# Kernel optimization log

Measured on AMD Instinct MI355X. Metric: run time of the kernel, lower is better.

## Reference

```python
import jax, jax.numpy as jnp
import numpy as np

B, N, L = 32, 50, 16384  # batch, n_templates, segment length
KT = 4096                # template kernel length


def conv1d(x, w, pad, groups=1):
    # x: [B, Cin, L], w: [Cout, Cin/groups, K] (torch layout)
    return jax.lax.conv_general_dilated(
        x, w, window_strides=(1,), padding=[(pad, pad)],
        dimension_numbers=('NCH', 'OIH', 'NCH'), feature_group_count=groups)


def maxpool3(x):
    # MaxPool1d(kernel=3, stride=3), floor mode (VALID)
    return jax.lax.reduce_window(x, -jnp.inf, jax.lax.max,
                                 (1, 1, 3), (1, 1, 3), 'VALID')


def pad_to(x, m):
    p = (-x.shape[-1]) % m
    pads = ((0, 0),) * (x.ndim - 1) + ((0, p),)
    return jnp.pad(x, pads)


def setup_inputs() -> dict:
    key = jax.random.key(0)
    ks = jax.random.split(key, 12)
    return dict(
        xi=jax.random.normal(ks[0], (B, 2, L), jnp.float32),
        S_t_m12=jax.random.normal(ks[1], (2, 1, L), jnp.float32) * 0.01,
        template=jax.random.normal(ks[2], (N, 2, KT), jnp.float32) * 0.01,
        hh_sqrt=jax.random.uniform(ks[3], (N, 2), jnp.float32) + 0.5,
        W1=jax.random.normal(ks[4], (16, 2, 3), jnp.float32) * 0.1,
        b1=jnp.zeros((16,), jnp.float32),
        W2=jax.random.normal(ks[5], (32, 16, 3), jnp.float32) * 0.1,
        b2=jnp.zeros((32,), jnp.float32),
        W3=jax.random.normal(ks[6], (32, 128), jnp.float32) * 0.1,
        b3=jnp.zeros((32,), jnp.float32),
        W4=jax.random.normal(ks[7], (2, 32), jnp.float32) * 0.1,
        b4=jnp.zeros((2,), jnp.float32),
    )


def reference(xi, S_t_m12, template, hh_sqrt, W1, b1, W2, b2, W3, b3, W4, b4):
    # Whitening matched filter: grouped conv with kernel length L
    y = conv1d(xi, S_t_m12, L - 1, groups=2)          # [B, 2, 2L-1]
    y = pad_to(y, L)                                   # [B, 2, 2L]
    # wrap-fold each channel: reshape(B,2,L).sum over the fold axis
    d_SA = y[:, 0].reshape(-1, 2, L).sum(1)[:, None, :]  # [B,1,L]
    d_SE = y[:, 1].reshape(-1, 2, L).sum(1)[:, None, :]
    h_SA = template[:, 0, :].reshape(-1, 1, KT)          # [N,1,KT]
    h_SE = template[:, 1, :].reshape(-1, 1, KT)
    dh_A = pad_to(conv1d(d_SA, h_SA, KT - 1), L).reshape(-1, N, 2, L).sum(2)  # [B,N,L]
    dh_E = pad_to(conv1d(d_SE, h_SE, KT - 1), L).reshape(-1, N, 2, L).sum(2)
    z = jnp.stack((dh_A, dh_E), -1).transpose(0, 2, 1, 3)  # [B,L,N,2]
    z = z / hh_sqrt                                         # broadcast [N,2]
    z = z.max(axis=1).transpose(0, 2, 1)                    # [B,2,N]
    # small CNN + MLP head
    h = maxpool3(jax.nn.sigmoid(conv1d(z, W1, 0) + b1[None, :, None]))  # [B,16,16]
    h = maxpool3(jax.nn.sigmoid(conv1d(h, W2, 0) + b2[None, :, None]))  # [B,32,4]
    h = h.reshape(h.shape[0], -1)                                        # [B,128]
    h = jax.nn.relu(h @ W3.T + b3)
    return h @ W4.T + b4                                                 # [B,2]
```

## Files before the change

kernel.cpp:

```cpp
#include <hip/hip_runtime.h>
#include <math.h>

#define L_LEN 16384
#define M_LEN 8192
#define KT_LEN 4096
#define BB 32
#define NTPL 50
#define SPEC_STRIDE 8224
#define NSIG 166
#define NT 512
#define PI_F 3.14159265358979323846f
#define C16 0.98078528040323044f
#define S16 0.19509032201612827f

typedef float cf2 __attribute__((ext_vector_type(2)));


__device__ __forceinline__ cf2 cmul(cf2 a, cf2 b) {
    cf2 byx = __builtin_shufflevector(b, b, 1, 0);
    return (cf2){a.x, a.x} * b + (cf2){-a.y, a.y} * byx;
}
__device__ __forceinline__ cf2 cmulc(cf2 a, cf2 b) {
    return a * (cf2){b.x, b.x} + (cf2){a.y, -a.x} * (cf2){b.y, b.y};
}
template<int SIGN>
__device__ __forceinline__ cf2 rot90(cf2 z) {
    return (SIGN < 0) ? (cf2){z.y, -z.x} : (cf2){-z.y, z.x};
}
template<int SIGN>
__device__ __forceinline__ cf2 ldT(const cf2* __restrict__ T, int idx) {
    cf2 t = T[idx];
    if (SIGN > 0) t.y = -t.y;
    return t;
}

__device__ __forceinline__ int swz(int i) { return i ^ (((i >> 5) & 15) << 1); }

__device__ __forceinline__ int pos(int f) {
    return ((f & 15) << 9) | (((f >> 4) & 15) << 5) |
           (((f >> 8) & 15) << 1) | ((f >> 12) & 1);
}

template<int SIGN>
__device__ __forceinline__ void dft16(cf2 x[16]) {
    const float S = (SIGN < 0) ? -1.f : 1.f;
    const cf2 w1 = {0.9238795325112867f, S * 0.3826834323650898f};
    const cf2 w2 = {0.7071067811865476f, S * 0.7071067811865476f};
    const cf2 w3 = {0.3826834323650898f, S * 0.9238795325112867f};
    cf2 v[16];
    #pragma unroll
    for (int n1 = 0; n1 < 4; ++n1) {
        cf2 a0 = x[n1], a1 = x[n1+4], a2 = x[n1+8], a3 = x[n1+12];
        cf2 t0 = a0 + a2, t2 = a0 - a2;
        cf2 t1 = a1 + a3, t3 = rot90<SIGN>(a1 - a3);
        cf2 u0 = t0 + t1, u1 = t2 + t3;
        cf2 u2 = t0 - t1, u3 = t2 - t3;
        if (n1 == 1) { u1 = cmul(u1, w1); u2 = cmul(u2, w2); u3 = cmul(u3, w3); }
        else if (n1 == 2) { u1 = cmul(u1, w2); u2 = rot90<SIGN>(u2);
                            u3 = rot90<SIGN>(cmul(u3, w2)); }
        else if (n1 == 3) { u1 = cmul(u1, w3); u2 = rot90<SIGN>(cmul(u2, w2));
                            u3 = -cmul(u3, w1); }
        v[0*4+n1] = u0; v[1*4+n1] = u1; v[2*4+n1] = u2; v[3*4+n1] = u3;
    }
    #pragma unroll
    for (int r = 0; r < 4; ++r) {
        cf2 a0 = v[r*4+0], a1 = v[r*4+1], a2 = v[r*4+2], a3 = v[r*4+3];
        cf2 t0 = a0 + a2, t2 = a0 - a2;
        cf2 t1 = a1 + a3, t3 = rot90<SIGN>(a1 - a3);
        x[r]    = t0 + t1; x[r+4]  = t2 + t3;
        x[r+8]  = t0 - t1; x[r+12] = t2 - t3;
    }
}

template<int SIGN>
__device__ __forceinline__ void butterfly16(cf2* A, const int idx[16], cf2 w1) {
    cf2 x[16];
    #pragma unroll
    for (int n = 0; n < 16; ++n) x[n] = A[idx[n]];
    dft16<SIGN>(x);
    A[idx[0]] = x[0];
    A[idx[1]] = cmul(x[1], w1);
    const cf2 w2 = cmul(w1, w1);
    A[idx[2]] = cmul(x[2], w2);
    const cf2 w3 = cmul(w1, w2);
    A[idx[3]] = cmul(x[3], w3);
    const cf2 w4 = cmul(w2, w2);
    A[idx[4]] = cmul(x[4], w4);
    A[idx[5]] = cmul(x[5], cmul(w1, w4));
    A[idx[6]] = cmul(x[6], cmul(w2, w4));
    A[idx[7]] = cmul(x[7], cmul(w3, w4));
    const cf2 w8 = cmul(w4, w4);
    A[idx[8]]  = cmul(x[8],  w8);
    A[idx[9]]  = cmul(x[9],  cmul(w1, w8));
    A[idx[10]] = cmul(x[10], cmul(w2, w8));
    A[idx[11]] = cmul(x[11], cmul(w3, w8));
    const cf2 w12 = cmul(w4, w8);
    A[idx[12]] = cmul(x[12], w12);
    A[idx[13]] = cmul(x[13], cmul(w1, w12));
    A[idx[14]] = cmul(x[14], cmul(w2, w12));
    A[idx[15]] = cmul(x[15], cmul(w3, w12));
}


__global__ __launch_bounds__(NT, 4)
void fwd_fft_kernel(const float* __restrict__ xi, const float* __restrict__ w,
                    const float* __restrict__ tmpl, cf2* __restrict__ Tw,
                    cf2* __restrict__ spec) {
    __shared__ __attribute__((aligned(16))) cf2 A[M_LEN];
    const int sig = blockIdx.x;
    const int tid = threadIdx.x;

    if (sig >= NSIG) {
        const int k = (sig - NSIG) * NT + tid;
        const double a = -M_PI * (double)k / 8192.0;
        Tw[k] = (cf2){(float)cos(a), (float)sin(a)};
        return;
    }

    const float* src;
    int nre;
    if (sig < 64)      { src = xi   + sig * L_LEN;         nre = L_LEN; }
    else if (sig < 66) { src = w    + (sig - 64) * L_LEN;  nre = L_LEN; }
    else               { src = tmpl + (sig - 66) * KT_LEN; nre = KT_LEN; }
    const bool isW = (sig >= 64 && sig < 66);
    const int nc = nre >> 1;
    const float4* s4 = (const float4*)src;
    const int g0 = tid ^ ((tid >> 4) & 15);
    #pragma unroll
    for (int m = 0; m < 8; ++m) {
        const int u = 2*tid + 1024*m;
        float4 vv = (u < nc) ? s4[tid + 512*m] : make_float4(0.f, 0.f, 0.f, 0.f);
        ((float4*)A)[g0 + 512*m] = vv;
    }
    __syncthreads();

    {
        int idx[16]; const int b0 = swz(tid);
        #pragma unroll
        for (int n = 0; n < 16; ++n) idx[n] = b0 + 512*n;
        float sn, cs; __sincosf(-PI_F * (float)(2*tid) / 8192.f, &sn, &cs);
        butterfly16<-1>(A, idx, (cf2){cs, sn});
    }
    __syncthreads();
    {
        const int blk = tid >> 5, j = tid & 31, jb = blk*512;
        int idx[16];
        #pragma unroll
        for (int n = 0; n < 16; ++n) idx[n] = jb + 32*n + (j ^ (2*n));
        float sn, cs; __sincosf(-PI_F * (float)(32*j) / 8192.f, &sn, &cs);
        butterfly16<-1>(A, idx, (cf2){cs, sn});
    }
    __syncthreads();
    {
        const int blk = tid >> 1, j = tid & 1;
        const int xv = (blk & 15) << 1, b3 = blk*32 + j;
        int idx[16];
        #pragma unroll
        for (int n = 0; n < 16; ++n) idx[n] = b3 + ((2*n) ^ xv);
        cf2 w1 = j ? (cf2){C16, -S16} : (cf2){1.f, 0.f};
        butterfly16<-1>(A, idx, w1);
    }
    __syncthreads();
    #pragma unroll
    for (int m = 0; m < 8; ++m) {
        float4 pq = ((float4*)A)[g0 + 512*m];
        ((float4*)A)[g0 + 512*m] = make_float4(pq.x + pq.z, pq.y + pq.w,
                                               pq.x - pq.z, pq.y - pq.w);
    }
    __syncthreads();

    cf2* out = spec + (size_t)sig * SPEC_STRIDE;
    #pragma unroll
    for (int m = 0; m < 16; ++m) {
        const int f = tid + 512*m;
        const int fb = (M_LEN - f) & (M_LEN - 1);
        cf2 Za = A[swz(pos(f))];
        cf2 Zb = A[swz(pos(fb))];
        cf2 E = (cf2){0.5f*(Za.x + Zb.x), 0.5f*(Za.y - Zb.y)};
        cf2 D = (cf2){Za.x - Zb.x, Za.y + Zb.y};
        cf2 O = (cf2){0.5f*D.y, -0.5f*D.x};
        float sn, cs;
        __sincosf(-PI_F * (float)f / 8192.f, &sn, &cs);
        cf2 val = E + (cf2){cs*O.x - sn*O.y, cs*O.y + sn*O.x};
        if (isW) {
            const int k = (4094 * f) & (L_LEN - 1);
            float psn, pcs; __sincosf(-PI_F * (float)k / 8192.f, &psn, &pcs);
            val = cmul((cf2){val.x, -val.y}, (cf2){pcs, psn});
        }
        out[f] = val;
    }
    if (tid == 0) {
        cf2 Za = A[swz(0)];
        cf2 val = (cf2){Za.x - Za.y, 0.f};
        if (isW) {
            val = (cf2){-val.x, 0.f};
        }
        out[M_LEN] = val;
    }
}

__global__ __launch_bounds__(NT, 4)
void inv_fft_kernel(const cf2* __restrict__ spec, const cf2* __restrict__ T,
                    const float* __restrict__ hh, float* __restrict__ zarr) {
    __shared__ __attribute__((aligned(16))) cf2 A[M_LEN];
    const int idx0 = blockIdx.x;
    const int c = idx0 & 1;
    const int n = (idx0 >> 1) % NTPL;
    const int b = idx0 / (2 * NTPL);
    const int tid = threadIdx.x;

    const cf2* Xs = spec + (size_t)(b*2 + c)      * SPEC_STRIDE;
    const cf2* Vs = spec + (size_t)(64 + c)       * SPEC_STRIDE;
    const cf2* Hs = spec + (size_t)(66 + n*2 + c) * SPEC_STRIDE;
    const float4* X4 = (const float4*)Xs;
    const float4* V4 = (const float4*)Vs;
    const float4* H4 = (const float4*)Hs;
    const float4* T4 = (const float4*)T;
    const int g0 = tid ^ ((tid >> 4) & 15);

    #pragma unroll
    for (int m = 0; m < 4; ++m) {
        const int u = 2*tid + 1024*m;
        float4 xf = X4[tid + 512*m], vf = V4[tid + 512*m], hf = H4[tid + 512*m];
        cf2 Sa0 = cmulc(cmul((cf2){xf.x, xf.y}, (cf2){vf.x, vf.y}), (cf2){hf.x, hf.y});
        cf2 Sa1 = cmulc(cmul((cf2){xf.z, xf.w}, (cf2){vf.z, vf.w}), (cf2){hf.z, hf.w});
        cf2 Sb0 = cmulc(cmul(Xs[M_LEN - u],     Vs[M_LEN - u]),     Hs[M_LEN - u]);
        cf2 Sb1 = cmulc(cmul(Xs[M_LEN - 1 - u], Vs[M_LEN - 1 - u]), Hs[M_LEN - 1 - u]);
        float4 tw = T4[tid + 512*m];
        float cs0 = tw.x, sn0 = -tw.y;
        float Ex0 = 0.5f*(Sa0.x + Sb0.x), Ey0 = 0.5f*(Sa0.y - Sb0.y);
        float Dx0 = Sa0.x - Sb0.x,        Dy0 = Sa0.y + Sb0.y;
        float Ox0 = 0.5f*(cs0*Dx0 - sn0*Dy0), Oy0 = 0.5f*(cs0*Dy0 + sn0*Dx0);
        float cs1 = tw.z, sn1 = -tw.w;
        float Ex1 = 0.5f*(Sa1.x + Sb1.x), Ey1 = 0.5f*(Sa1.y - Sb1.y);
        float Dx1 = Sa1.x - Sb1.x,        Dy1 = Sa1.y + Sb1.y;
        float Ox1 = 0.5f*(cs1*Dx1 - sn1*Dy1), Oy1 = 0.5f*(cs1*Dy1 + sn1*Dx1);
        ((float4*)A)[g0 + 512*m] = make_float4(Ex0 - Oy0, Ey0 + Ox0,
                                               Ex1 - Oy1, Ey1 + Ox1);
        if (u > 0) A[swz(M_LEN - u)] = (cf2){Ex0 + Oy0, Ox0 - Ey0};
        A[swz(M_LEN - 1 - u)] = (cf2){Ex1 + Oy1, Ox1 - Ey1};
    }
    if (tid == 0) {
        cf2 S = cmulc(cmul(Xs[4096], Vs[4096]), Hs[4096]);
        A[swz(4096)] = (cf2){S.x, -S.y};
    }
    __syncthreads();

    {
        int idx[16]; const int b0 = swz(tid);
        #pragma unroll
        for (int nn = 0; nn < 16; ++nn) idx[nn] = b0 + 512*nn;
        butterfly16<+1>(A, idx, ldT<+1>(T, 2*tid));
    }
    __syncthreads();
    {
        const int blk = tid >> 5, j = tid & 31, jb = blk*512;
        int idx[16];
        #pragma unroll
        for (int nn = 0; nn < 16; ++nn) idx[nn] = jb + 32*nn + (j ^ (2*nn));
        butterfly16<+1>(A, idx, ldT<+1>(T, 32*j));
    }
    __syncthreads();
    {
        const int blk = tid >> 1, j = tid & 1;
        const int xv = (blk & 15) << 1, b3 = blk*32 + j;
        int idx[16];
        #pragma unroll
        for (int nn = 0; nn < 16; ++nn) idx[nn] = b3 + ((2*nn) ^ xv);
        cf2 w1 = j ? (cf2){C16, S16} : (cf2){1.f, 0.f};
        butterfly16<+1>(A, idx, w1);
    }
    __syncthreads();

    float mx = -INFINITY;
    #pragma unroll
    for (int m = 0; m < 8; ++m) {
        float4 pq = ((const float4*)A)[g0 + 512*m];
        mx = fmaxf(mx, fmaxf(fmaxf(pq.x + pq.z, pq.y + pq.w),
                             fmaxf(pq.x - pq.z, pq.y - pq.w)));
    }
    __syncthreads();
    for (int off = 32; off > 0; off >>= 1)
        mx = fmaxf(mx, __shfl_xor(mx, off));
    const int lane = tid & 63, wv = tid >> 6;
    float* redf = (float*)A;
    if (lane == 0) redf[wv] = mx;
    __syncthreads();
    if (tid == 0) {
        float mm = redf[0];
        for (int i = 1; i < NT/64; ++i) mm = fmaxf(mm, redf[i]);
        zarr[(b*2 + c)*NTPL + n] = mm / ((float)M_LEN * hh[n*2 + c]);
    }
}

__global__ __launch_bounds__(256)
void head_kernel(const float* __restrict__ zarr,
                 const float* __restrict__ W1, const float* __restrict__ b1,
                 const float* __restrict__ W2, const float* __restrict__ b2,
                 const float* __restrict__ W3, const float* __restrict__ b3,
                 const float* __restrict__ W4, const float* __restrict__ b4,
                 float* __restrict__ out) {
    __shared__ float zl[2][NTPL];
    __shared__ float s1[16][48];
    __shared__ float p1[16][16];
    __shared__ float s2[32][14];
    __shared__ float hflat[128];
    __shared__ float h1[32];
    const int b = blockIdx.x, tid = threadIdx.x;

    for (int i = tid; i < 2*NTPL; i += 256) zl[i/NTPL][i%NTPL] = zarr[b*2*NTPL + i];
    __syncthreads();
    for (int i = tid; i < 16*48; i += 256) {
        const int o = i / 48, t = i % 48;
        float acc = b1[o];
        #pragma unroll
        for (int cc = 0; cc < 2; ++cc)
            #pragma unroll
            for (int k = 0; k < 3; ++k)
                acc += zl[cc][t+k] * W1[o*6 + cc*3 + k];
        s1[o][t] = 1.f / (1.f + __expf(-acc));
    }
    __syncthreads();
    for (int i = tid; i < 16*16; i += 256) {
        const int o = i / 16, u = i % 16;
        p1[o][u] = fmaxf(fmaxf(s1[o][3*u], s1[o][3*u+1]), s1[o][3*u+2]);
    }
    __syncthreads();
    for (int i = tid; i < 32*14; i += 256) {
        const int o = i / 14, t = i % 14;
        float acc = b2[o];
        for (int cc = 0; cc < 16; ++cc)
            #pragma unroll
            for (int k = 0; k < 3; ++k)
                acc += p1[cc][t+k] * W2[o*48 + cc*3 + k];
        s2[o][t] = 1.f / (1.f + __expf(-acc));
    }
    __syncthreads();
    for (int i = tid; i < 128; i += 256) {
        const int o = i / 4, u = i % 4;
        hflat[i] = fmaxf(fmaxf(s2[o][3*u], s2[o][3*u+1]), s2[o][3*u+2]);
    }
    __syncthreads();
    if (tid < 32) {
        float acc = b3[tid];
        for (int j = 0; j < 128; ++j) acc += hflat[j] * W3[tid*128 + j];
        h1[tid] = fmaxf(acc, 0.f);
    }
    __syncthreads();
    if (tid < 2) {
        float acc = b4[tid];
        for (int j = 0; j < 32; ++j) acc += h1[j] * W4[tid*32 + j];
        out[b*2 + tid] = acc;
    }
}

extern "C" void kernel_launch(void* const* d_in, const int* in_sizes, int n_in,
                              void* d_out, int out_size, void* d_ws, size_t ws_size,
                              hipStream_t stream) {
    const float* xi   = (const float*)d_in[0];
    const float* Sw   = (const float*)d_in[1];
    const float* tmpl = (const float*)d_in[2];
    const float* hh   = (const float*)d_in[3];
    const float* W1   = (const float*)d_in[4];
    const float* b1   = (const float*)d_in[5];
    const float* W2   = (const float*)d_in[6];
    const float* b2   = (const float*)d_in[7];
    const float* W3   = (const float*)d_in[8];
    const float* b3   = (const float*)d_in[9];
    const float* W4   = (const float*)d_in[10];
    const float* b4   = (const float*)d_in[11];
    float* out = (float*)d_out;

    cf2* T16  = (cf2*)d_ws;
    cf2* spec = T16 + 16384;
    float* zarr = (float*)(spec + (size_t)NSIG * SPEC_STRIDE);

    fwd_fft_kernel<<<dim3(NSIG + 32), dim3(NT), 0, stream>>>(xi, Sw, tmpl, T16, spec);
    inv_fft_kernel<<<dim3(BB * NTPL * 2), dim3(NT), 0, stream>>>(spec, T16, hh, zarr);
    head_kernel<<<dim3(BB), dim3(256), 0, stream>>>(zarr, W1, b1, W2, b2, W3, b3, W4, b4, out);
}
```

Before: 160.4 us.

## Switch 8192-point FFTs from radix-16 to radix-8 with 1024 threads

Restructures the shared-memory FFT from three radix-16 passes over 512 threads into four radix-8 passes over 1024 threads, with new index swizzles and output bit-reversal mapping. The aim is to cut per-thread register pressure and raise occupancy and parallelism per block. In exchange it adds an extra pass and barrier per FFT. The twiddle table is now built with fast float sincos and quadrant symmetry instead of double-precision cos/sin, which may reduce its accuracy slightly.

```diff
diff --git a/kernel.cpp b/kernel.cpp
--- a/kernel.cpp
+++ b/kernel.cpp
@@ -8,10 +8,10 @@
 #define NTPL 50
 #define SPEC_STRIDE 8224
 #define NSIG 166
-#define NT 512
+#define NT 1024
 #define PI_F 3.14159265358979323846f
-#define C16 0.98078528040323044f
-#define S16 0.19509032201612827f
+#define C8 0.92387953251128674f
+#define S8 0.38268343236508978f
 
 typedef float cf2 __attribute__((ext_vector_type(2)));
 
@@ -36,48 +36,35 @@
 
 __device__ __forceinline__ int swz(int i) { return i ^ (((i >> 5) & 15) << 1); }
 
-__device__ __forceinline__ int pos(int f) {
-    return ((f & 15) << 9) | (((f >> 4) & 15) << 5) |
-           (((f >> 8) & 15) << 1) | ((f >> 12) & 1);
+__device__ __forceinline__ int pos8(int f) {
+    return ((f & 7) << 10) | (((f >> 3) & 7) << 7) |
+           (((f >> 6) & 7) << 4) | (((f >> 9) & 7) << 1) | ((f >> 12) & 1);
 }
 
 template<int SIGN>
-__device__ __forceinline__ void dft16(cf2 x[16]) {
-    const float S = (SIGN < 0) ? -1.f : 1.f;
-    const cf2 w1 = {0.9238795325112867f, S * 0.3826834323650898f};
-    const cf2 w2 = {0.7071067811865476f, S * 0.7071067811865476f};
-    const cf2 w3 = {0.3826834323650898f, S * 0.9238795325112867f};
-    cf2 v[16];
-    #pragma unroll
-    for (int n1 = 0; n1 < 4; ++n1) {
-        cf2 a0 = x[n1], a1 = x[n1+4], a2 = x[n1+8], a3 = x[n1+12];
-        cf2 t0 = a0 + a2, t2 = a0 - a2;
-        cf2 t1 = a1 + a3, t3 = rot90<SIGN>(a1 - a3);
-        cf2 u0 = t0 + t1, u1 = t2 + t3;
-        cf2 u2 = t0 - t1, u3 = t2 - t3;
-        if (n1 == 1) { u1 = cmul(u1, w1); u2 = cmul(u2, w2); u3 = cmul(u3, w3); }
-        else if (n1 == 2) { u1 = cmul(u1, w2); u2 = rot90<SIGN>(u2);
-                            u3 = rot90<SIGN>(cmul(u3, w2)); }
-        else if (n1 == 3) { u1 = cmul(u1, w3); u2 = rot90<SIGN>(cmul(u2, w2));
-                            u3 = -cmul(u3, w1); }
-        v[0*4+n1] = u0; v[1*4+n1] = u1; v[2*4+n1] = u2; v[3*4+n1] = u3;
-    }
-    #pragma unroll
-    for (int r = 0; r < 4; ++r) {
-        cf2 a0 = v[r*4+0], a1 = v[r*4+1], a2 = v[r*4+2], a3 = v[r*4+3];
-        cf2 t0 = a0 + a2, t2 = a0 - a2;
-        cf2 t1 = a1 + a3, t3 = rot90<SIGN>(a1 - a3);
-        x[r]    = t0 + t1; x[r+4]  = t2 + t3;
-        x[r+8]  = t0 - t1; x[r+12] = t2 - t3;
-    }
+__device__ __forceinline__ void dft8(cf2 x[8]) {
+    const float R2 = 0.70710678118654752f;
+    const cf2 w81 = { R2, SIGN * R2 };
+    const cf2 w83 = { -R2, SIGN * R2 };
+    cf2 u0 = x[0] + x[4], u1 = x[1] + x[5], u2 = x[2] + x[6], u3 = x[3] + x[7];
+    cf2 v0 = x[0] - x[4];
+    cf2 v1 = cmul(x[1] - x[5], w81);
+    cf2 v2 = rot90<SIGN>(x[2] - x[6]);
+    cf2 v3 = cmul(x[3] - x[7], w83);
+    cf2 t0 = u0 + u2, t2 = u0 - u2;
+    cf2 t1 = u1 + u3, t3 = rot90<SIGN>(u1 - u3);
+    x[0] = t0 + t1; x[2] = t2 + t3; x[4] = t0 - t1; x[6] = t2 - t3;
+    cf2 s0 = v0 + v2, s2 = v0 - v2;
+    cf2 s1 = v1 + v3, s3 = rot90<SIGN>(v1 - v3);
+    x[1] = s0 + s1; x[3] = s2 + s3; x[5] = s0 - s1; x[7] = s2 - s3;
 }
 
 template<int SIGN>
-__device__ __forceinline__ void butterfly16(cf2* A, const int idx[16], cf2 w1) {
-    cf2 x[16];
-    #pragma unroll
-    for (int n = 0; n < 16; ++n) x[n] = A[idx[n]];
-    dft16<SIGN>(x);
+__device__ __forceinline__ void butterfly8(cf2* A, const int idx[8], cf2 w1) {
+    cf2 x[8];
+    #pragma unroll
+    for (int n = 0; n < 8; ++n) x[n] = A[idx[n]];
+    dft8<SIGN>(x);
     A[idx[0]] = x[0];
     A[idx[1]] = cmul(x[1], w1);
     const cf2 w2 = cmul(w1, w1);
@@ -89,20 +76,10 @@
     A[idx[5]] = cmul(x[5], cmul(w1, w4));
     A[idx[6]] = cmul(x[6], cmul(w2, w4));
     A[idx[7]] = cmul(x[7], cmul(w3, w4));
-    const cf2 w8 = cmul(w4, w4);
-    A[idx[8]]  = cmul(x[8],  w8);
-    A[idx[9]]  = cmul(x[9],  cmul(w1, w8));
-    A[idx[10]] = cmul(x[10], cmul(w2, w8));
-    A[idx[11]] = cmul(x[11], cmul(w3, w8));
-    const cf2 w12 = cmul(w4, w8);
-    A[idx[12]] = cmul(x[12], w12);
-    A[idx[13]] = cmul(x[13], cmul(w1, w12));
-    A[idx[14]] = cmul(x[14], cmul(w2, w12));
-    A[idx[15]] = cmul(x[15], cmul(w3, w12));
-}
-
-
-__global__ __launch_bounds__(NT, 4)
+}
+
+
+__global__ __launch_bounds__(NT, 8)
 void fwd_fft_kernel(const float* __restrict__ xi, const float* __restrict__ w,
                     const float* __restrict__ tmpl, cf2* __restrict__ Tw,
                     cf2* __restrict__ spec) {
@@ -112,8 +89,14 @@
 
     if (sig >= NSIG) {
         const int k = (sig - NSIG) * NT + tid;
-        const double a = -M_PI * (double)k / 8192.0;
-        Tw[k] = (cf2){(float)cos(a), (float)sin(a)};
+        const int quad = k >> 12, mm = k & 4095;
+        float s, c; __sincosf(PI_F * (float)mm / 8192.f, &s, &c);
+        cf2 v;
+        if      (quad == 0) v = (cf2){ c, -s};
+        else if (quad == 1) v = (cf2){-s, -c};
+        else if (quad == 2) v = (cf2){-c,  s};
+        else                v = (cf2){ s,  c};
+        Tw[k] = v;
         return;
     }
 
@@ -127,55 +110,68 @@
     const float4* s4 = (const float4*)src;
     const int g0 = tid ^ ((tid >> 4) & 15);
     #pragma unroll
+    for (int m = 0; m < 4; ++m) {
+        const int u = 2*tid + 2048*m;
+        float4 vv = (u < nc) ? s4[tid + 1024*m] : make_float4(0.f, 0.f, 0.f, 0.f);
+        ((float4*)A)[g0 + 1024*m] = vv;
+    }
+    __syncthreads();
+
+    {
+        int idx[8]; const int b0 = swz(tid);
+        #pragma unroll
+        for (int n = 0; n < 8; ++n) idx[n] = b0 + 1024*n;
+        float sn, cs; __sincosf(-PI_F * (float)(2*tid) / 8192.f, &sn, &cs);
+        butterfly8<-1>(A, idx, (cf2){cs, sn});
+    }
+    __syncthreads();
+    {
+        const int blk = tid >> 7, j = tid & 127, jb = blk*1024;
+        const int jsw = j ^ (((j >> 5) & 3) << 1);
+        int idx[8];
+        #pragma unroll
+        for (int n = 0; n < 8; ++n) idx[n] = jb + 128*n + (jsw ^ ((n & 3) << 3));
+        float sn, cs; __sincosf(-PI_F * (float)(16*j) / 8192.f, &sn, &cs);
+        butterfly8<-1>(A, idx, (cf2){cs, sn});
+    }
+    __syncthreads();
+    {
+        const int blk = tid >> 4, j = tid & 15;
+        const int base = blk*128 + j, bx = (blk & 3) << 3;
+        int idx[8];
+        #pragma unroll
+        for (int n = 0; n < 8; ++n) idx[n] = (base + 16*n) ^ bx ^ ((n >> 1) << 1);
+        float sn, cs; __sincosf(-PI_F * (float)(128*j) / 8192.f, &sn, &cs);
+        butterfly8<-1>(A, idx, (cf2){cs, sn});
+    }
+    __syncthreads();
+    {
+        const int blk = tid >> 1, j = tid & 1;
+        const int Xa = ((blk >> 1) & 15) << 1;
+        const int base = ((blk << 4) | j) ^ (Xa & 16);
+        const int xv = Xa & 14;
+        int idx[8];
+        #pragma unroll
+        for (int n = 0; n < 8; ++n) idx[n] = base + ((2*n) ^ xv);
+        cf2 w1 = j ? (cf2){C8, -S8} : (cf2){1.f, 0.f};
+        butterfly8<-1>(A, idx, w1);
+    }
+    __syncthreads();
+    #pragma unroll
+    for (int m = 0; m < 4; ++m) {
+        float4 pq = ((float4*)A)[g0 + 1024*m];
+        ((float4*)A)[g0 + 1024*m] = make_float4(pq.x + pq.z, pq.y + pq.w,
+                                                pq.x - pq.z, pq.y - pq.w);
+    }
+    __syncthreads();
+
+    cf2* out = spec + (size_t)sig * SPEC_STRIDE;
+    #pragma unroll
     for (int m = 0; m < 8; ++m) {
-        const int u = 2*tid + 1024*m;
-        float4 vv = (u < nc) ? s4[tid + 512*m] : make_float4(0.f, 0.f, 0.f, 0.f);
-        ((float4*)A)[g0 + 512*m] = vv;
-    }
-    __syncthreads();
-
-    {
-        int idx[16]; const int b0 = swz(tid);
-        #pragma unroll
-        for (int n = 0; n < 16; ++n) idx[n] = b0 + 512*n;
-        float sn, cs; __sincosf(-PI_F * (float)(2*tid) / 8192.f, &sn, &cs);
-        butterfly16<-1>(A, idx, (cf2){cs, sn});
-    }
-    __syncthreads();
-    {
-        const int blk = tid >> 5, j = tid & 31, jb = blk*512;
-        int idx[16];
-        #pragma unroll
-        for (int n = 0; n < 16; ++n) idx[n] = jb + 32*n + (j ^ (2*n));
-        float sn, cs; __sincosf(-PI_F * (float)(32*j) / 8192.f, &sn, &cs);
-        butterfly16<-1>(A, idx, (cf2){cs, sn});
-    }
-    __syncthreads();
-    {
-        const int blk = tid >> 1, j = tid & 1;
-        const int xv = (blk & 15) << 1, b3 = blk*32 + j;
-        int idx[16];
-        #pragma unroll
-        for (int n = 0; n < 16; ++n) idx[n] = b3 + ((2*n) ^ xv);
-        cf2 w1 = j ? (cf2){C16, -S16} : (cf2){1.f, 0.f};
-        butterfly16<-1>(A, idx, w1);
-    }
-    __syncthreads();
-    #pragma unroll
-    for (int m = 0; m < 8; ++m) {
-        float4 pq = ((float4*)A)[g0 + 512*m];
-        ((float4*)A)[g0 + 512*m] = make_float4(pq.x + pq.z, pq.y + pq.w,
-                                               pq.x - pq.z, pq.y - pq.w);
-    }
-    __syncthreads();
-
-    cf2* out = spec + (size_t)sig * SPEC_STRIDE;
-    #pragma unroll
-    for (int m = 0; m < 16; ++m) {
-        const int f = tid + 512*m;
+        const int f = tid + 1024*m;
         const int fb = (M_LEN - f) & (M_LEN - 1);
-        cf2 Za = A[swz(pos(f))];
-        cf2 Zb = A[swz(pos(fb))];
+        cf2 Za = A[swz(pos8(f))];
+        cf2 Zb = A[swz(pos8(fb))];
         cf2 E = (cf2){0.5f*(Za.x + Zb.x), 0.5f*(Za.y - Zb.y)};
         cf2 D = (cf2){Za.x - Zb.x, Za.y + Zb.y};
         cf2 O = (cf2){0.5f*D.y, -0.5f*D.x};
@@ -199,7 +195,7 @@
     }
 }
 
-__global__ __launch_bounds__(NT, 4)
+__global__ __launch_bounds__(NT, 8)
 void inv_fft_kernel(const cf2* __restrict__ spec, const cf2* __restrict__ T,
                     const float* __restrict__ hh, float* __restrict__ zarr) {
     __shared__ __attribute__((aligned(16))) cf2 A[M_LEN];
@@ -219,14 +215,14 @@
     const int g0 = tid ^ ((tid >> 4) & 15);
 
     #pragma unroll
-    for (int m = 0; m < 4; ++m) {
-        const int u = 2*tid + 1024*m;
-        float4 xf = X4[tid + 512*m], vf = V4[tid + 512*m], hf = H4[tid + 512*m];
+    for (int m = 0; m < 2; ++m) {
+        const int u = 2*tid + 2048*m;
+        float4 xf = X4[tid + 1024*m], vf = V4[tid + 1024*m], hf = H4[tid + 1024*m];
         cf2 Sa0 = cmulc(cmul((cf2){xf.x, xf.y}, (cf2){vf.x, vf.y}), (cf2){hf.x, hf.y});
         cf2 Sa1 = cmulc(cmul((cf2){xf.z, xf.w}, (cf2){vf.z, vf.w}), (cf2){hf.z, hf.w});
         cf2 Sb0 = cmulc(cmul(Xs[M_LEN - u],     Vs[M_LEN - u]),     Hs[M_LEN - u]);
         cf2 Sb1 = cmulc(cmul(Xs[M_LEN - 1 - u], Vs[M_LEN - 1 - u]), Hs[M_LEN - 1 - u]);
-        float4 tw = T4[tid + 512*m];
+        float4 tw = T4[tid + 1024*m];
         float cs0 = tw.x, sn0 = -tw.y;
         float Ex0 = 0.5f*(Sa0.x + Sb0.x), Ey0 = 0.5f*(Sa0.y - Sb0.y);
         float Dx0 = Sa0.x - Sb0.x,        Dy0 = Sa0.y + Sb0.y;
@@ -235,8 +231,8 @@
         float Ex1 = 0.5f*(Sa1.x + Sb1.x), Ey1 = 0.5f*(Sa1.y - Sb1.y);
         float Dx1 = Sa1.x - Sb1.x,        Dy1 = Sa1.y + Sb1.y;
         float Ox1 = 0.5f*(cs1*Dx1 - sn1*Dy1), Oy1 = 0.5f*(cs1*Dy1 + sn1*Dx1);
-        ((float4*)A)[g0 + 512*m] = make_float4(Ex0 - Oy0, Ey0 + Ox0,
-                                               Ex1 - Oy1, Ey1 + Ox1);
+        ((float4*)A)[g0 + 1024*m] = make_float4(Ex0 - Oy0, Ey0 + Ox0,
+                                                Ex1 - Oy1, Ey1 + Ox1);
         if (u > 0) A[swz(M_LEN - u)] = (cf2){Ex0 + Oy0, Ox0 - Ey0};
         A[swz(M_LEN - 1 - u)] = (cf2){Ex1 + Oy1, Ox1 - Ey1};
     }
@@ -247,35 +243,47 @@
     __syncthreads();
 
     {
-        int idx[16]; const int b0 = swz(tid);
-        #pragma unroll
-        for (int nn = 0; nn < 16; ++nn) idx[nn] = b0 + 512*nn;
-        butterfly16<+1>(A, idx, ldT<+1>(T, 2*tid));
-    }
-    __syncthreads();
-    {
-        const int blk = tid >> 5, j = tid & 31, jb = blk*512;
-        int idx[16];
-        #pragma unroll
-        for (int nn = 0; nn < 16; ++nn) idx[nn] = jb + 32*nn + (j ^ (2*nn));
-        butterfly16<+1>(A, idx, ldT<+1>(T, 32*j));
+        int idx[8]; const int b0 = swz(tid);
+        #pragma unroll
+        for (int nn = 0; nn < 8; ++nn) idx[nn] = b0 + 1024*nn;
+        butterfly8<+1>(A, idx, ldT<+1>(T, 2*tid));
+    }
+    __syncthreads();
+    {
+        const int blk = tid >> 7, j = tid & 127, jb = blk*1024;
+        const int jsw = j ^ (((j >> 5) & 3) << 1);
+        int idx[8];
+        #pragma unroll
+        for (int nn = 0; nn < 8; ++nn) idx[nn] = jb + 128*nn + (jsw ^ ((nn & 3) << 3));
+        butterfly8<+1>(A, idx, ldT<+1>(T, 16*j));
+    }
+    __syncthreads();
+    {
+        const int blk = tid >> 4, j = tid & 15;
+        const int base = blk*128 + j, bx = (blk & 3) << 3;
+        int idx[8];
+        #pragma unroll
+        for (int nn = 0; nn < 8; ++nn) idx[nn] = (base + 16*nn) ^ bx ^ ((nn >> 1) << 1);
+        butterfly8<+1>(A, idx, ldT<+1>(T, 128*j));
     }
     __syncthreads();
     {
         const int blk = tid >> 1, j = tid & 1;
-        const int xv = (blk & 15) << 1, b3 = blk*32 + j;
-        int idx[16];
-        #pragma unroll
-        for (int nn = 0; nn < 16; ++nn) idx[nn] = b3 + ((2*nn) ^ xv);
-        cf2 w1 = j ? (cf2){C16, S16} : (cf2){1.f, 0.f};
-        butterfly16<+1>(A, idx, w1);
+        const int Xa = ((blk >> 1) & 15) << 1;
+        const int base = ((blk << 4) | j) ^ (Xa & 16);
+        const int xv = Xa & 14;
+        int idx[8];
+        #pragma unroll
+        for (int nn = 0; nn < 8; ++nn) idx[nn] = base + ((2*nn) ^ xv);
+        cf2 w1 = j ? (cf2){C8, S8} : (cf2){1.f, 0.f};
+        butterfly8<+1>(A, idx, w1);
     }
     __syncthreads();
 
     float mx = -INFINITY;
     #pragma unroll
-    for (int m = 0; m < 8; ++m) {
-        float4 pq = ((const float4*)A)[g0 + 512*m];
+    for (int m = 0; m < 4; ++m) {
+        float4 pq = ((const float4*)A)[g0 + 1024*m];
         mx = fmaxf(mx, fmaxf(fmaxf(pq.x + pq.z, pq.y + pq.w),
                              fmaxf(pq.x - pq.z, pq.y - pq.w)));
     }
@@ -375,7 +383,7 @@
     cf2* spec = T16 + 16384;
     float* zarr = (float*)(spec + (size_t)NSIG * SPEC_STRIDE);
 
-    fwd_fft_kernel<<<dim3(NSIG + 32), dim3(NT), 0, stream>>>(xi, Sw, tmpl, T16, spec);
+    fwd_fft_kernel<<<dim3(NSIG + 16), dim3(NT), 0, stream>>>(xi, Sw, tmpl, T16, spec);
     inv_fft_kernel<<<dim3(BB * NTPL * 2), dim3(NT), 0, stream>>>(spec, T16, hh, zarr);
     head_kernel<<<dim3(BB), dim3(256), 0, stream>>>(zarr, W1, b1, W2, b2, W3, b3, W4, b4, out);
 }
```

Result: no change. 162.3 us (+1.2%).
